# Kernel tuning notes

Measured on AMD Instinct MI355X. Metric: run time of the kernel, lower is better.

## Reference

```python
import jax, jax.numpy as jnp
import numpy as np

T_OBS, T_PRE, B, IN, E, H = 8, 12, 524288, 2, 16, 8


def setup_inputs() -> dict:
    key = jax.random.key(0)
    ks = jax.random.split(key, 16)
    s = 0.25  # small init scale for weights
    d = {
        "obs_traj_rel": jax.random.normal(ks[0], (T_OBS, B, IN), jnp.float32),
        "pre_traj_rel": jax.random.normal(ks[1], (T_PRE, B, IN), jnp.float32),
        "h0": jax.random.normal(ks[2], (B, H), jnp.float32),
        "c0": jax.random.normal(ks[3], (B, H), jnp.float32),
        "c0_pre": jax.random.normal(ks[4], (B, H), jnp.float32),
        "W_in": jax.random.normal(ks[5], (E, IN), jnp.float32) * s,
        "b_in": jax.random.normal(ks[6], (E,), jnp.float32) * s,
        "W_ih_obs": jax.random.normal(ks[7], (4 * H, E), jnp.float32) * s,
        "W_hh_obs": jax.random.normal(ks[8], (4 * H, H), jnp.float32) * s,
        "b_ih_obs": jax.random.normal(ks[9], (4 * H,), jnp.float32) * s,
        "b_hh_obs": jax.random.normal(ks[10], (4 * H,), jnp.float32) * s,
        "W_ih_pre": jax.random.normal(ks[11], (4 * H, E), jnp.float32) * s,
        "W_hh_pre": jax.random.normal(ks[12], (4 * H, H), jnp.float32) * s,
        "b_ih_pre": jax.random.normal(ks[13], (4 * H,), jnp.float32) * s,
        "b_hh_pre": jax.random.normal(ks[14], (4 * H,), jnp.float32) * s,
    }
    return d


def _lstm_scan(emb, h, c, W_ih, W_hh, b_ih, b_hh):
    """emb: [T, B, E]; PyTorch LSTMCell gate order i, f, g, o."""
    b = b_ih + b_hh

    def step(carry, x):
        h, c = carry
        gates = x @ W_ih.T + h @ W_hh.T + b  # [B, 4H]
        i, f, g, o = jnp.split(gates, 4, axis=-1)
        c = jax.nn.sigmoid(f) * c + jax.nn.sigmoid(i) * jnp.tanh(g)
        h = jax.nn.sigmoid(o) * jnp.tanh(c)
        return (h, c), None

    (h, c), _ = jax.lax.scan(step, (h, c), emb)
    return h, c


def reference(obs_traj_rel, pre_traj_rel, h0, c0, c0_pre,
              W_in, b_in,
              W_ih_obs, W_hh_obs, b_ih_obs, b_hh_obs,
              W_ih_pre, W_hh_pre, b_ih_pre, b_hh_pre):
    batch = obs_traj_rel.shape[1]
    # shared input embedding layer applied to all timesteps at once
    emb_obs = obs_traj_rel @ W_in.T + b_in  # [T_obs, B, E]
    h, c = _lstm_scan(emb_obs, h0, c0, W_ih_obs, W_hh_obs, b_ih_obs, b_hh_obs)
    # faithful to original: permute(1,0).reshape(batch, -1) == transpose then reshape
    c_out = jnp.transpose(h).reshape(batch, -1)
    emb_pre = pre_traj_rel @ W_in.T + b_in  # [T_pre, B, E]
    # hidden_h carries over from obs loop; cell state re-initialized (c0_pre)
    h2, _ = _lstm_scan(emb_pre, h, c0_pre, W_ih_pre, W_hh_pre, b_ih_pre, b_hh_pre)
    x_out = jnp.transpose(h2).reshape(batch, -1)
    return (c_out, x_out)
```

## Files before the change

### kernel.cpp

```cpp
#include <hip/hip_runtime.h>
#include <stdint.h>

#define T_OBS 8
#define T_PRE 12
#define BATCH 524288

#define NLOG2E  (-1.4426950408889634f)
#define P2LOG2E ( 2.8853900817779268f)

typedef __fp16 half8  __attribute__((ext_vector_type(8)));
typedef float  floatx16 __attribute__((ext_vector_type(16)));
typedef unsigned int uint_t;

__device__ __forceinline__ uint_t upk(float a, float b) {
    return __builtin_bit_cast(uint_t, __builtin_amdgcn_cvt_pkrtz(a, b));
}

__global__ void prep_weights(const float* __restrict__ W_in,
                             const float* __restrict__ b_in,
                             const float* __restrict__ W_ih_obs,
                             const float* __restrict__ W_hh_obs,
                             const float* __restrict__ b_ih_obs,
                             const float* __restrict__ b_hh_obs,
                             const float* __restrict__ W_ih_pre,
                             const float* __restrict__ W_hh_pre,
                             const float* __restrict__ b_ih_pre,
                             const float* __restrict__ b_hh_pre,
                             uint_t* __restrict__ wsu) {
    int t = threadIdx.x;
    int phase = t >> 6;
    int l = t & 63;
    int m = l & 31;
    int kh = l >> 5;
    const float* W_ih = phase ? W_ih_pre : W_ih_obs;
    const float* W_hh = phase ? W_hh_pre : W_hh_obs;
    const float* b_ih = phase ? b_ih_pre : b_ih_obs;
    const float* b_hh = phase ? b_hh_pre : b_hh_obs;

    float wx0 = 0.f, wx1 = 0.f;
    float bb = b_ih[m] + b_hh[m];
    #pragma unroll
    for (int e = 0; e < 16; e++) {
        float wie = W_ih[m * 16 + e];
        wx0 += wie * W_in[e * 2 + 0];
        wx1 += wie * W_in[e * 2 + 1];
        bb  += wie * b_in[e];
    }
    float s = (m >= 16 && m < 24) ? P2LOG2E : NLOG2E;

    float af[16];
    af[0] = wx0 * s;
    af[1] = wx1 * s;
    #pragma unroll
    for (int j = 0; j < 8; j++) af[2 + j] = W_hh[m * 8 + j] * s;
    af[10] = bb * s;
    #pragma unroll
    for (int k = 11; k < 16; k++) af[k] = 0.f;

    #pragma unroll
    for (int r = 0; r < 4; r++)
        wsu[phase * 256 + l * 4 + r] = upk(af[kh * 8 + 2 * r], af[kh * 8 + 2 * r + 1]);
}

__device__ __forceinline__ void lstm_step(half8 A, uint_t xpk, bool lo,
                                          uint_t& pk0, uint_t& pk1,
                                          float c[4], float h[4],
                                          const floatx16& zacc) {
    uint_t other = (uint_t)__shfl_xor((int)pk0, 32, 64);
    uint4 bu;
    bu.x = lo ? xpk : pk1;
    bu.y = lo ? pk0 : 0x00003C00u;
    bu.z = lo ? pk1 : 0u;
    bu.w = lo ? other : 0u;
    half8 B = __builtin_bit_cast(half8, bu);

    floatx16 d = __builtin_amdgcn_mfma_f32_32x32x16_f16(A, B, zacc, 0, 0, 0);

    #pragma unroll
    for (int j = 0; j < 4; j++) {
        float gi = d[j], gf = d[4 + j], gg = d[8 + j], go = d[12 + j];
        float si = __builtin_amdgcn_rcpf(1.f + __builtin_amdgcn_exp2f(gi));
        float sf = __builtin_amdgcn_rcpf(1.f + __builtin_amdgcn_exp2f(gf));
        float so = __builtin_amdgcn_rcpf(1.f + __builtin_amdgcn_exp2f(go));
        float tg = 1.f - 2.f * __builtin_amdgcn_rcpf(1.f + __builtin_amdgcn_exp2f(gg));
        float cn = sf * c[j] + si * tg;
        c[j] = cn;
        float tc = 1.f - 2.f * __builtin_amdgcn_rcpf(1.f + __builtin_amdgcn_exp2f(P2LOG2E * cn));
        h[j] = so * tc;
    }
    pk0 = upk(h[0], h[1]);
    pk1 = upk(h[2], h[3]);
}

__global__ __launch_bounds__(256, 2)
void lstm_encoder(const float2* __restrict__ obs,
                  const float2* __restrict__ pre,
                  const float4* __restrict__ h0,
                  const float4* __restrict__ c0,
                  const float4* __restrict__ c0p,
                  const uint4* __restrict__ wf,
                  float* __restrict__ out) {
    const int tid  = threadIdx.x;
    const int lane = tid & 63;
    const int wv   = tid >> 6;
    const int n    = lane & 31;
    const int half = lane >> 5;
    const bool lo  = (half == 0);
    const size_t nb = (size_t)blockIdx.x * 128 + wv * 32 + n;

    half8 Aobs = __builtin_bit_cast(half8, wf[lane]);
    half8 Apre = __builtin_bit_cast(half8, wf[64 + lane]);

    floatx16 zacc;
    #pragma unroll
    for (int i = 0; i < 16; i++) zacc[i] = 0.f;

    float4 hv = h0[nb * 2 + half];
    float4 cv = c0[nb * 2 + half];
    float c[4] = {cv.x, cv.y, cv.z, cv.w};
    float h[4] = {hv.x, hv.y, hv.z, hv.w};
    uint_t pk0 = upk(h[0], h[1]);
    uint_t pk1 = upk(h[2], h[3]);

    #pragma unroll 1
    for (int t = 0; t < T_OBS; t++) {
        float2 xv = obs[(size_t)t * BATCH + nb];
        lstm_step(Aobs, upk(xv.x, xv.y), lo, pk0, pk1, c, h, zacc);
    }

    #pragma unroll
    for (int j = 0; j < 4; j++)
        out[(size_t)(half * 4 + j) * BATCH + nb] = h[j];

    float4 cv2 = c0p[nb * 2 + half];
    c[0] = cv2.x; c[1] = cv2.y; c[2] = cv2.z; c[3] = cv2.w;

    #pragma unroll 1
    for (int t = 0; t < T_PRE; t++) {
        float2 xv = pre[(size_t)t * BATCH + nb];
        lstm_step(Apre, upk(xv.x, xv.y), lo, pk0, pk1, c, h, zacc);
    }

    #pragma unroll
    for (int j = 0; j < 4; j++)
        out[(size_t)(8 + half * 4 + j) * BATCH + nb] = h[j];
}

extern "C" void kernel_launch(void* const* d_in, const int* in_sizes, int n_in,
                              void* d_out, int out_size, void* d_ws, size_t ws_size,
                              hipStream_t stream) {
    prep_weights<<<1, 128, 0, stream>>>(
        (const float*)d_in[5],  (const float*)d_in[6],
        (const float*)d_in[7],  (const float*)d_in[8],
        (const float*)d_in[9],  (const float*)d_in[10],
        (const float*)d_in[11], (const float*)d_in[12],
        (const float*)d_in[13], (const float*)d_in[14],
        (uint_t*)d_ws);

    lstm_encoder<<<BATCH / 128, 256, 0, stream>>>(
        (const float2*)d_in[0], (const float2*)d_in[1],
        (const float4*)d_in[2], (const float4*)d_in[3], (const float4*)d_in[4],
        (const uint4*)d_ws, (float*)d_out);
}
```

Baseline: 229.4 us.

## Split K across lane halves to drop shuffle, fuse gate reciprocals, prefetch inputs

Rearranges the MFMA weight layout so each lane half supplies its own hidden values, with the x and bias terms halved and duplicated across both halves. This removes the cross-half shuffle and the per-lane selects. It also merges the sigmoid and tanh reciprocals algebraically, cutting five rcp per element down to two. The next timestep's input is loaded one step ahead and the c0_pre load is hoisted. The merged exp/product forms risk overflow to inf for large gate pre-activations.

Measured after the change: 218.6 us. 4.7% less time.

```diff
diff --git a/kernel.cpp b/kernel.cpp
--- a/kernel.cpp
+++ b/kernel.cpp
@@ -49,44 +49,53 @@
     float s = (m >= 16 && m < 24) ? P2LOG2E : NLOG2E;
 
     float af[16];
-    af[0] = wx0 * s;
-    af[1] = wx1 * s;
+    af[0] = wx0 * s * 0.5f;
+    af[1] = wx1 * s * 0.5f;
     #pragma unroll
-    for (int j = 0; j < 8; j++) af[2 + j] = W_hh[m * 8 + j] * s;
-    af[10] = bb * s;
+    for (int j = 0; j < 4; j++) af[2 + j] = W_hh[m * 8 + j] * s;
+    af[6] = bb * s * 0.5f;
+    af[7] = 0.f;
+    af[8] = af[0];
+    af[9] = af[1];
     #pragma unroll
-    for (int k = 11; k < 16; k++) af[k] = 0.f;
+    for (int j = 0; j < 4; j++) af[10 + j] = W_hh[m * 8 + 4 + j] * s;
+    af[14] = af[6];
+    af[15] = 0.f;
 
     #pragma unroll
     for (int r = 0; r < 4; r++)
         wsu[phase * 256 + l * 4 + r] = upk(af[kh * 8 + 2 * r], af[kh * 8 + 2 * r + 1]);
 }
 
-__device__ __forceinline__ void lstm_step(half8 A, uint_t xpk, bool lo,
+__device__ __forceinline__ void lstm_step(half8 A, uint_t xpk,
                                           uint_t& pk0, uint_t& pk1,
                                           float c[4], float h[4],
                                           const floatx16& zacc) {
-    uint_t other = (uint_t)__shfl_xor((int)pk0, 32, 64);
     uint4 bu;
-    bu.x = lo ? xpk : pk1;
-    bu.y = lo ? pk0 : 0x00003C00u;
-    bu.z = lo ? pk1 : 0u;
-    bu.w = lo ? other : 0u;
+    bu.x = xpk;
+    bu.y = pk0;
+    bu.z = pk1;
+    bu.w = 0x00003C00u;
     half8 B = __builtin_bit_cast(half8, bu);
 
     floatx16 d = __builtin_amdgcn_mfma_f32_32x32x16_f16(A, B, zacc, 0, 0, 0);
 
     #pragma unroll
     for (int j = 0; j < 4; j++) {
-        float gi = d[j], gf = d[4 + j], gg = d[8 + j], go = d[12 + j];
-        float si = __builtin_amdgcn_rcpf(1.f + __builtin_amdgcn_exp2f(gi));
-        float sf = __builtin_amdgcn_rcpf(1.f + __builtin_amdgcn_exp2f(gf));
-        float so = __builtin_amdgcn_rcpf(1.f + __builtin_amdgcn_exp2f(go));
-        float tg = 1.f - 2.f * __builtin_amdgcn_rcpf(1.f + __builtin_amdgcn_exp2f(gg));
-        float cn = sf * c[j] + si * tg;
+        float ei = __builtin_amdgcn_exp2f(d[j]);
+        float ef = __builtin_amdgcn_exp2f(d[4 + j]);
+        float eg = __builtin_amdgcn_exp2f(d[8 + j]);
+        float eo = __builtin_amdgcn_exp2f(d[12 + j]);
+        float ai  = 1.f + ei;
+        float afv = 1.f + ef;
+        float ag  = 1.f + eg;
+        float gm  = eg - 1.f;
+        float p   = ai * ag;
+        float num = __builtin_fmaf(c[j], p, gm * afv);
+        float cn  = num * __builtin_amdgcn_rcpf(p * afv);
         c[j] = cn;
-        float tc = 1.f - 2.f * __builtin_amdgcn_rcpf(1.f + __builtin_amdgcn_exp2f(P2LOG2E * cn));
-        h[j] = so * tc;
+        float ec = __builtin_amdgcn_exp2f(P2LOG2E * cn);
+        h[j] = (ec - 1.f) * __builtin_amdgcn_rcpf((1.f + eo) * (1.f + ec));
     }
     pk0 = upk(h[0], h[1]);
     pk1 = upk(h[2], h[3]);
@@ -105,7 +114,6 @@
     const int wv   = tid >> 6;
     const int n    = lane & 31;
     const int half = lane >> 5;
-    const bool lo  = (half == 0);
     const size_t nb = (size_t)blockIdx.x * 128 + wv * 32 + n;
 
     half8 Aobs = __builtin_bit_cast(half8, wf[lane]);
@@ -115,31 +123,40 @@
     #pragma unroll
     for (int i = 0; i < 16; i++) zacc[i] = 0.f;
 
-    float4 hv = h0[nb * 2 + half];
-    float4 cv = c0[nb * 2 + half];
+    float4 hv  = h0[nb * 2 + half];
+    float4 cv  = c0[nb * 2 + half];
+    float4 cv2 = c0p[nb * 2 + half];
     float c[4] = {cv.x, cv.y, cv.z, cv.w};
     float h[4] = {hv.x, hv.y, hv.z, hv.w};
     uint_t pk0 = upk(h[0], h[1]);
     uint_t pk1 = upk(h[2], h[3]);
 
+    float2 xv = obs[nb];
     #pragma unroll 1
-    for (int t = 0; t < T_OBS; t++) {
-        float2 xv = obs[(size_t)t * BATCH + nb];
-        lstm_step(Aobs, upk(xv.x, xv.y), lo, pk0, pk1, c, h, zacc);
+    for (int t = 0; t < T_OBS - 1; t++) {
+        float2 xn = obs[(size_t)(t + 1) * BATCH + nb];
+        lstm_step(Aobs, upk(xv.x, xv.y), pk0, pk1, c, h, zacc);
+        xv = xn;
+    }
+    {
+        float2 xn = pre[nb];
+        lstm_step(Aobs, upk(xv.x, xv.y), pk0, pk1, c, h, zacc);
+        xv = xn;
     }
 
     #pragma unroll
     for (int j = 0; j < 4; j++)
         out[(size_t)(half * 4 + j) * BATCH + nb] = h[j];
 
-    float4 cv2 = c0p[nb * 2 + half];
     c[0] = cv2.x; c[1] = cv2.y; c[2] = cv2.z; c[3] = cv2.w;
 
     #pragma unroll 1
-    for (int t = 0; t < T_PRE; t++) {
-        float2 xv = pre[(size_t)t * BATCH + nb];
-        lstm_step(Apre, upk(xv.x, xv.y), lo, pk0, pk1, c, h, zacc);
+    for (int t = 0; t < T_PRE - 1; t++) {
+        float2 xn = pre[(size_t)(t + 1) * BATCH + nb];
+        lstm_step(Apre, upk(xv.x, xv.y), pk0, pk1, c, h, zacc);
+        xv = xn;
     }
+    lstm_step(Apre, upk(xv.x, xv.y), pk0, pk1, c, h, zacc);
 
     #pragma unroll
     for (int j = 0; j < 4; j++)
```
